# Performance work log

Measured on AMD Instinct MI355X. Metric: run time of the kernel, lower is better.

Reference implementation:

```python
import jax, jax.numpy as jnp
import numpy as np


def setup_inputs() -> dict:
    key = jax.random.key(0)
    k1, k2 = jax.random.split(key)
    B, C, H, W = 8, 64, 64, 64
    x = jax.random.normal(k1, (B, C, H, W), dtype=jnp.float32)
    stdv = 1.0 / np.sqrt(C)
    weight = jax.random.uniform(k2, (C, C), dtype=jnp.float32, minval=-stdv, maxval=stdv)
    return {"x": x, "weight": weight}


def reference(x, weight):
    B, C, H, W = x.shape
    N = H * W
    xf = x.reshape(B, C, N)            # [B, C, N]
    g_x = jnp.transpose(xf, (0, 2, 1))  # [B, N, C] (also theta_x)
    # f[b, i, j] = sum_c x[b, c, i] * x[b, c, j]
    f = jnp.einsum('bic,bcj->bij', g_x, xf)  # [B, N, N]
    adj = jax.nn.softmax(f, axis=-1)
    support = jnp.einsum('bnc,cd->bnd', g_x, weight)  # [B, N, C]
    y = jnp.einsum('bij,bjc->bic', adj, support)      # [B, N, C]
    y = jnp.transpose(y, (0, 2, 1)).reshape(B, C, H, W)
    return y + x
```

## Files before the change

kernel.cpp:

```cpp
#include <hip/hip_runtime.h>
#include <stdint.h>


#define NTOK 4096
#define CCH  64

typedef float v4f __attribute__((ext_vector_type(4)));
typedef __bf16 v8bf __attribute__((ext_vector_type(8)));
typedef unsigned short v8us __attribute__((ext_vector_type(8)));
typedef __fp16 v2fp __attribute__((ext_vector_type(2)));
typedef _Float16 v8h __attribute__((ext_vector_type(8)));

__device__ __forceinline__ unsigned short f2bf(float f) {
    union { float f; unsigned int u; } c; c.f = f;
    unsigned int r = c.u + 0x7fffu + ((c.u >> 16) & 1u);
    return (unsigned short)(r >> 16);
}

__device__ __forceinline__ v8bf ld8(const unsigned short* p) {
    union { v8us s; v8bf b; } u;
    u.s = *(const v8us*)p;
    return u.b;
}

__device__ __forceinline__ unsigned int pkbf(float a, float b) {
    union { float f; unsigned int u; } ua, ub; ua.f = a; ub.f = b;
    return __builtin_amdgcn_perm(ub.u, ua.u, 0x07060302u);
}

__device__ __forceinline__ float ex2(float x) {
#if __has_builtin(__builtin_amdgcn_exp2f)
    return __builtin_amdgcn_exp2f(x);
#else
    return exp2f(x);
#endif
}

__device__ __forceinline__ void gload_lds16(const void* g, void* l) {
    __builtin_amdgcn_global_load_lds(
        (const __attribute__((address_space(1))) unsigned int*)g,
        (__attribute__((address_space(3))) unsigned int*)l,
        16, 0, 0);
}

__global__ __launch_bounds__(256) void prep_kernel(
    const float* __restrict__ x,
    const float* __restrict__ w,
    unsigned short* __restrict__ xT,
    unsigned short* __restrict__ sT)
{
    __shared__ float Xf[64 * 65];

    const int tid  = threadIdx.x;
    const int lane = tid & 63;
    const int wv   = __builtin_amdgcn_readfirstlane(tid >> 6);
    const int b    = blockIdx.y;
    const int n0   = blockIdx.x * 64;

    const float* xb = x + (size_t)b * CCH * NTOK + n0 + lane;
    #pragma unroll
    for (int k = 0; k < 16; ++k) {
        const int c = wv * 16 + k;
        Xf[c * 65 + lane] = xb[(size_t)c * NTOK];
    }
    __syncthreads();

    {
        const int n  = tid >> 2;
        const int c0 = (tid & 3) * 16;
        unsigned int pk[8];
        #pragma unroll
        for (int k = 0; k < 8; ++k) {
            const float a = Xf[(c0 + 2 * k) * 65 + n];
            const float c2 = Xf[(c0 + 2 * k + 1) * 65 + n];
            pk[k] = (unsigned int)f2bf(a) | ((unsigned int)f2bf(c2) << 16);
        }
        unsigned short* xtr = xT + ((size_t)b * NTOK + n0 + n) * CCH + c0;
        *(uint4*)(xtr)     = *(uint4*)(pk);
        *(uint4*)(xtr + 8) = *(uint4*)(pk + 4);
    }

    float acc[16];
    #pragma unroll
    for (int d = 0; d < 16; ++d) acc[d] = 0.f;

    #pragma unroll 4
    for (int c = 0; c < 64; ++c) {
        const float xc = Xf[c * 65 + lane];
        const float* wr = w + c * 64 + wv * 16;
        #pragma unroll
        for (int d = 0; d < 16; ++d) acc[d] = fmaf(xc, wr[d], acc[d]);
    }
    unsigned short* stb = sT + (size_t)b * CCH * NTOK + n0 + lane;
    #pragma unroll
    for (int d = 0; d < 16; ++d)
        stb[(size_t)(wv * 16 + d) * NTOK] = f2bf(acc[d]);
}

__global__ __launch_bounds__(256, 4) void flash_kernel(
    const unsigned short* __restrict__ xT,
    const unsigned short* __restrict__ sT,
    unsigned short* __restrict__ part_o,
    float* __restrict__ part_l,
    int nchunk, int chunk_len)
{
    __shared__ __align__(16) unsigned short Kt[2][64 * 64];
    __shared__ __align__(16) unsigned short Vt[2][64 * 64];

    const int tid  = threadIdx.x;
    const int w    = tid >> 6;
    const int lane = tid & 63;
    const int quad = lane >> 4;
    const int l16  = lane & 15;
    const int l7   = l16 & 7;
    const int b     = blockIdx.z;
    const int chunk = blockIdx.y;
    const int i0   = blockIdx.x * 128;
    const int irow = i0 + w * 32;
    const int jb   = chunk * chunk_len;

    const unsigned short* xTb = xT + (size_t)b * NTOK * CCH;
    const unsigned short* sTb = sT + (size_t)b * CCH * NTOK;

    const int srow = w * 8 + (lane >> 3);
    const int sc   = (lane & 7) ^ (lane >> 3);
    const int ksrow = 8 * ((srow & 12) >> 2) + 4 * ((srow >> 4) & 1) + (srow & 3);

    auto stage = [&](int j0, int bf) {
        unsigned short* kd = Kt[bf] + w * 512;
        unsigned short* vd = Vt[bf] + w * 512;
        gload_lds16(xTb + (size_t)(j0 + ksrow) * CCH + sc * 8,       kd);
        gload_lds16(xTb + (size_t)(j0 + 32 + ksrow) * CCH + sc * 8,  kd + 2048);
        gload_lds16(sTb + (size_t)srow * NTOK + j0 + sc * 8,        vd);
        gload_lds16(sTb + (size_t)(32 + srow) * NTOK + j0 + sc * 8, vd + 2048);
    };

    stage(jb, 0);

    v8bf aq0[2], aq1[2];
    #pragma unroll
    for (int m = 0; m < 2; ++m) {
        const unsigned short* qr = xTb + (size_t)(irow + m * 16 + l16) * CCH + quad * 8;
        aq0[m] = ld8(qr);
        aq1[m] = ld8(qr + 32);
    }

    const float L2E = 1.4426950408889634f;
    float negm2[2];
    #pragma unroll
    for (int m = 0; m < 2; ++m) {
        float msq = 0.f;
        #pragma unroll
        for (int i = 0; i < 8; ++i) {
            float e0 = (float)aq0[m][i], e1 = (float)aq1[m][i];
            msq = fmaf(e0, e0, msq);
            msq = fmaf(e1, e1, msq);
        }
        msq += __shfl_xor(msq, 16);
        msq += __shfl_xor(msq, 32);
        negm2[m] = -msq * L2E;
    }

    #pragma unroll
    for (int m = 0; m < 2; ++m)
        #pragma unroll
        for (int i = 0; i < 8; ++i) {
            aq0[m][i] = (__bf16)((float)aq0[m][i] * L2E);
            aq1[m][i] = (__bf16)((float)aq1[m][i] * L2E);
        }

    v4f zini[2];
    #pragma unroll
    for (int m = 0; m < 2; ++m) {
        zini[m][0] = negm2[m]; zini[m][1] = negm2[m];
        zini[m][2] = negm2[m]; zini[m][3] = negm2[m];
    }

    v4f o[2][4];
    #pragma unroll
    for (int m = 0; m < 2; ++m)
        #pragma unroll
        for (int ct = 0; ct < 4; ++ct) { o[m][ct][0]=0.f; o[m][ct][1]=0.f; o[m][ct][2]=0.f; o[m][ct][3]=0.f; }
    float rsum[2] = {0.f, 0.f};

    const int koffA = l16 * 64 + (quad ^ l7) * 8;
    const int koffB = koffA ^ 32;

    auto compute = [&](const unsigned short* Kc, const unsigned short* Vc) {
        #pragma unroll
        for (int h = 0; h < 2; ++h) {
            uint2 pk[2][2];
            #pragma unroll
            for (int jtl = 0; jtl < 2; ++jtl) {
                const int kb = h * 2048 + jtl * 1024;
                v8bf bk0 = ld8(Kc + kb + koffA);
                v8bf bk1 = ld8(Kc + kb + koffB);
                #pragma unroll
                for (int m = 0; m < 2; ++m) {
                    v4f z;
                    z = __builtin_amdgcn_mfma_f32_16x16x32_bf16(bk0, aq0[m], zini[m], 0, 0, 0);
                    z = __builtin_amdgcn_mfma_f32_16x16x32_bf16(bk1, aq1[m], z, 0, 0, 0);
                    const float p0 = ex2(z[0]);
                    const float p1 = ex2(z[1]);
                    const float p2 = ex2(z[2]);
                    const float p3 = ex2(z[3]);
                    rsum[m] += (p0 + p1) + (p2 + p3);
                    pk[m][jtl].x = pkbf(p0, p1);
                    pk[m][jtl].y = pkbf(p2, p3);
                }
            }

            union { unsigned int u[4]; v8bf bv8; } pb[2];
            #pragma unroll
            for (int m = 0; m < 2; ++m) {
                pb[m].u[0] = pk[m][0].x; pb[m].u[1] = pk[m][0].y;
                pb[m].u[2] = pk[m][1].x; pb[m].u[3] = pk[m][1].y;
            }

            #pragma unroll
            for (int ct = 0; ct < 4; ++ct) {
                v8bf bv = ld8(Vc + ct * 1024 + (h == 0 ? koffA : koffB));
                #pragma unroll
                for (int m = 0; m < 2; ++m)
                    o[m][ct] = __builtin_amdgcn_mfma_f32_16x16x32_bf16(bv, pb[m].bv8, o[m][ct], 0, 0, 0);
            }
        }
    };

    for (int jj = 0; jj < chunk_len; jj += 128) {
        __syncthreads();
        stage(jb + jj + 64, 1);
        compute(Kt[0], Vt[0]);
        __syncthreads();
        if (jj + 128 < chunk_len)
            stage(jb + jj + 128, 0);
        compute(Kt[1], Vt[1]);
    }

    const size_t pbase = (size_t)(b * nchunk + chunk) * NTOK + irow;
    #pragma unroll
    for (int m = 0; m < 2; ++m) {
        float t = rsum[m];
        t += __shfl_xor(t, 16);
        t += __shfl_xor(t, 32);
        if (quad == 0) part_l[pbase + m * 16 + l16] = t;
    }
    unsigned short* po = part_o + pbase * 64;
    #pragma unroll
    for (int m = 0; m < 2; ++m)
        #pragma unroll
        for (int ct = 0; ct < 4; ++ct) {
            union { struct { v2fp a, b; } h; uint2 u; } cv;
            cv.h.a = __builtin_amdgcn_cvt_pkrtz(o[m][ct][0], o[m][ct][1]);
            cv.h.b = __builtin_amdgcn_cvt_pkrtz(o[m][ct][2], o[m][ct][3]);
            *(uint2*)(po + (size_t)(m * 16 + l16) * 64 + ct * 16 + quad * 4) = cv.u;
        }
}

__global__ __launch_bounds__(256) void combine_kernel(
    const unsigned short* __restrict__ part_o,
    const float* __restrict__ part_l,
    const float* __restrict__ x,
    float* __restrict__ out,
    int nchunk)
{
    __shared__ float Of[64 * 65];
    const int tid = threadIdx.x;
    const int b = blockIdx.y;
    const int i0 = blockIdx.x * 64;
    const int row = tid >> 2;
    const int seg = tid & 3;

    float acc[16];
    #pragma unroll
    for (int k = 0; k < 16; ++k) acc[k] = 0.f;
    float lt = 0.f;

    auto body = [&](int ch) {
        const size_t base = (size_t)(b * nchunk + ch) * NTOK + i0 + row;
        lt += part_l[base];
        const unsigned short* po = part_o + base * 64 + seg * 16;
        v8h a = *(const v8h*)(po);
        v8h c2 = *(const v8h*)(po + 8);
        #pragma unroll
        for (int k = 0; k < 8; ++k) {
            acc[k]     += (float)a[k];
            acc[8 + k] += (float)c2[k];
        }
    };
    if (nchunk == 4) { body(0); body(1); body(2); body(3); }
    else { for (int ch = 0; ch < nchunk; ++ch) body(ch); }

    const float inv = 1.f / lt;
    #pragma unroll
    for (int k = 0; k < 16; ++k) Of[row * 65 + seg * 16 + k] = acc[k] * inv;
    __syncthreads();

    const int c    = tid >> 2;
    const int part = tid & 3;
    const float* xrow = x   + ((size_t)b * CCH + c) * NTOK + i0 + part * 16;
    float*       orow = out + ((size_t)b * CCH + c) * NTOK + i0 + part * 16;
    #pragma unroll
    for (int i4 = 0; i4 < 4; ++i4) {
        float4 xv = *(const float4*)(xrow + i4 * 4);
        float4 ov;
        ov.x = Of[(part * 16 + i4 * 4 + 0) * 65 + c] + xv.x;
        ov.y = Of[(part * 16 + i4 * 4 + 1) * 65 + c] + xv.y;
        ov.z = Of[(part * 16 + i4 * 4 + 2) * 65 + c] + xv.z;
        ov.w = Of[(part * 16 + i4 * 4 + 3) * 65 + c] + xv.w;
        *(float4*)(orow + i4 * 4) = ov;
    }
}

extern "C" void kernel_launch(void* const* d_in, const int* in_sizes, int n_in,
                              void* d_out, int out_size, void* d_ws, size_t ws_size,
                              hipStream_t stream) {
    const float* x = (const float*)d_in[0];
    const float* w = (const float*)d_in[1];
    float* out = (float*)d_out;

    const size_t xT_elems = (size_t)8 * NTOK * CCH;
    unsigned short* xT = (unsigned short*)d_ws;
    unsigned short* sT = xT + xT_elems;
    char* rest = (char*)d_ws + 2 * xT_elems * sizeof(unsigned short);

    int KS = 4;
    while (KS > 1) {
        size_t need = 2 * xT_elems * sizeof(unsigned short)
                    + (size_t)KS * ((size_t)8 * NTOK * CCH * 2 + (size_t)8 * NTOK * 4);
        if (need <= ws_size) break;
        KS >>= 1;
    }
    unsigned short* part_o = (unsigned short*)rest;
    float* part_l = (float*)(rest + (size_t)KS * 8 * NTOK * CCH * 2);

    dim3 gp(64, 8);
    prep_kernel<<<gp, 256, 0, stream>>>(x, w, xT, sT);
    dim3 gf(32, KS, 8);
    flash_kernel<<<gf, 256, 0, stream>>>(xT, sT, part_o, part_l, KS, NTOK / KS);
    dim3 gc(64, 8);
    combine_kernel<<<gc, 256, 0, stream>>>(part_o, part_l, x, out, KS);
}
```

Before: 113.3 us.

## Compute softmax row sums via MFMA with ones and coalesce support stores

The per-element VALU row-sum accumulation of exponentiated scores is replaced with an extra MFMA that multiplies a ones vector by the packed bf16 probabilities, and the final cross-lane shuffles are dropped. The support-projection kernel now stages its results through shared memory so each thread writes 16 contiguous bf16 values instead of scattered 2-byte stores. This frees VALU cycles in the flash inner loop and improves store coalescing. The trade-off is extra matrix-unit work, that the row sums are now taken from bf16-rounded probabilities rather than fp32 ones, and two extra barriers in the projection kernel.

```diff
diff --git a/kernel.cpp b/kernel.cpp
--- a/kernel.cpp
+++ b/kernel.cpp
@@ -91,10 +91,26 @@
         #pragma unroll
         for (int d = 0; d < 16; ++d) acc[d] = fmaf(xc, wr[d], acc[d]);
     }
-    unsigned short* stb = sT + (size_t)b * CCH * NTOK + n0 + lane;
+
+    __syncthreads();
     #pragma unroll
     for (int d = 0; d < 16; ++d)
-        stb[(size_t)(wv * 16 + d) * NTOK] = f2bf(acc[d]);
+        Xf[(wv * 16 + d) * 65 + lane] = acc[d];
+    __syncthreads();
+    {
+        const int d   = tid >> 2;
+        const int prt = tid & 3;
+        const float* src = Xf + d * 65 + prt * 16;
+        unsigned int pk2[8];
+        #pragma unroll
+        for (int k = 0; k < 8; ++k)
+            pk2[k] = (unsigned int)f2bf(src[2 * k])
+                   | ((unsigned int)f2bf(src[2 * k + 1]) << 16);
+        unsigned short* dst = sT + (size_t)b * CCH * NTOK
+                            + (size_t)d * NTOK + n0 + prt * 16;
+        *(uint4*)(dst)     = *(uint4*)(pk2);
+        *(uint4*)(dst + 8) = *(uint4*)(pk2 + 4);
+    }
 }
 
 __global__ __launch_bounds__(256, 4) void flash_kernel(
@@ -176,12 +192,18 @@
         zini[m][2] = negm2[m]; zini[m][3] = negm2[m];
     }
 
+    v8bf ones;
+    #pragma unroll
+    for (int i = 0; i < 8; ++i) ones[i] = (__bf16)1.0f;
+
     v4f o[2][4];
     #pragma unroll
     for (int m = 0; m < 2; ++m)
         #pragma unroll
         for (int ct = 0; ct < 4; ++ct) { o[m][ct][0]=0.f; o[m][ct][1]=0.f; o[m][ct][2]=0.f; o[m][ct][3]=0.f; }
-    float rsum[2] = {0.f, 0.f};
+    v4f racc[2];
+    #pragma unroll
+    for (int m = 0; m < 2; ++m) { racc[m][0]=0.f; racc[m][1]=0.f; racc[m][2]=0.f; racc[m][3]=0.f; }
 
     const int koffA = l16 * 64 + (quad ^ l7) * 8;
     const int koffB = koffA ^ 32;
@@ -204,7 +226,6 @@
                     const float p1 = ex2(z[1]);
                     const float p2 = ex2(z[2]);
                     const float p3 = ex2(z[3]);
-                    rsum[m] += (p0 + p1) + (p2 + p3);
                     pk[m][jtl].x = pkbf(p0, p1);
                     pk[m][jtl].y = pkbf(p2, p3);
                 }
@@ -216,6 +237,10 @@
                 pb[m].u[0] = pk[m][0].x; pb[m].u[1] = pk[m][0].y;
                 pb[m].u[2] = pk[m][1].x; pb[m].u[3] = pk[m][1].y;
             }
+
+            #pragma unroll
+            for (int m = 0; m < 2; ++m)
+                racc[m] = __builtin_amdgcn_mfma_f32_16x16x32_bf16(ones, pb[m].bv8, racc[m], 0, 0, 0);
 
             #pragma unroll
             for (int ct = 0; ct < 4; ++ct) {
@@ -238,12 +263,9 @@
     }
 
     const size_t pbase = (size_t)(b * nchunk + chunk) * NTOK + irow;
-    #pragma unroll
-    for (int m = 0; m < 2; ++m) {
-        float t = rsum[m];
-        t += __shfl_xor(t, 16);
-        t += __shfl_xor(t, 32);
-        if (quad == 0) part_l[pbase + m * 16 + l16] = t;
+    if (quad == 0) {
+        part_l[pbase + l16]      = racc[0][0];
+        part_l[pbase + 16 + l16] = racc[1][0];
     }
     unsigned short* po = part_o + pbase * 64;
     #pragma unroll
```

Result: no change. 112.8 us (-0.5%).
